# Optimization experiments

Hardware: AMD Instinct MI355X
Metric: run time of the kernel (lower is better)

The kernel has to match this reference:

```python
import jax, jax.numpy as jnp
import numpy as np

T, D, DFF, E, K = 2048, 1024, 2816, 8, 2


def setup_inputs() -> dict:
    key = jax.random.key(0)
    k1, k2, k3, k4, k5, k6 = jax.random.split(key, 6)
    return {
        "x": jax.random.normal(k1, (T, D), dtype=jnp.float32),
        "topk_weight": jax.random.uniform(k2, (T, K), dtype=jnp.float32),
        "gate_w": jax.random.normal(k3, (E, DFF, D), dtype=jnp.float32) * 0.02,
        "up_w": jax.random.normal(k4, (E, DFF, D), dtype=jnp.float32) * 0.02,
        "down_w": jax.random.normal(k5, (E, D, DFF), dtype=jnp.float32) * 0.02,
        "topk_ids": jax.random.randint(k6, (T, K), 0, E, dtype=jnp.int64),
    }


def reference(x, topk_weight, gate_w, up_w, down_w, topk_ids):
    # x: [T, D]; topk_ids/topk_weight: [T, K]
    # Per expert: SwiGLU MLP over all tokens, combined with the per-token
    # routing weight for that expert (0 if the expert was not selected).
    out = jnp.zeros_like(x)
    num_experts = gate_w.shape[0]
    for e in range(num_experts):
        h = jax.nn.silu(x @ gate_w[e].T) * (x @ up_w[e].T)  # [T, DFF]
        y = h @ down_w[e].T                                  # [T, D]
        # sum over top-k slots of routing weight where this expert was chosen
        w_e = jnp.sum(jnp.where(topk_ids == e, topk_weight, 0.0), axis=1)  # [T]
        out = out + y * w_e[:, None]
    return out
```

## Files before the change

### kernel.cpp

```cpp
#include <hip/hip_runtime.h>
#include <stdint.h>

typedef __attribute__((ext_vector_type(8))) __bf16 bf16x8;
typedef __attribute__((ext_vector_type(4))) float f32x4;
typedef __attribute__((ext_vector_type(8))) unsigned short ushort8;

#define T_TOK 2048
#define D_DIM 1024
#define DFF   2816
#define NEXP  8
#define NROWS 4096
#define BK    32
#define NW_ELEM (NEXP * DFF * D_DIM)
#define MAXTM2 24

#define SWZ(r,g) ((g) ^ (((r) >> 1) & 3))

#define TL_N    0
#define TL_BASE 16
#define TL_VAL  80
#define TL_EXP  144

__device__ __forceinline__ void lds_cp16(const void* g, void* l) {
  __builtin_amdgcn_global_load_lds(
      (const __attribute__((address_space(1))) void*)g,
      (__attribute__((address_space(3))) void*)l, 16, 0, 0);
}

__device__ __forceinline__ ushort8 pack_bf16x8(float4 a, float4 b) {
  union { __bf16 h[8]; ushort8 u; } r;
  r.h[0] = (__bf16)a.x; r.h[1] = (__bf16)a.y; r.h[2] = (__bf16)a.z; r.h[3] = (__bf16)a.w;
  r.h[4] = (__bf16)b.x; r.h[5] = (__bf16)b.y; r.h[6] = (__bf16)b.z; r.h[7] = (__bf16)b.w;
  return r.u;
}

__device__ __forceinline__ unsigned short f2bf(float f) {
  union { __bf16 h; unsigned short u; } r;
  r.h = (__bf16)f;
  return r.u;
}

__device__ __forceinline__ float bf2f(unsigned short u) {
  union { uint32_t u; float f; } v; v.u = (uint32_t)u << 16;
  return v.f;
}

__device__ __forceinline__ int xcd_chunk(int bid, int nwork) {
  const int q = nwork >> 3, r = nwork & 7;
  const int xcd = bid & 7;
  const int base = (xcd < r) ? xcd * (q + 1) : r * (q + 1) + (xcd - r) * q;
  return base + (bid >> 3);
}

__global__ __launch_bounds__(512) void routing_kernel(
    const int* __restrict__ ids, const float* __restrict__ w,
    int* __restrict__ cnt, int* __restrict__ off,
    int* __restrict__ tok, float* __restrict__ wgt, int* __restrict__ rowmap,
    int* __restrict__ tl2)
{
  __shared__ int s_cnt[NEXP];
  __shared__ int s_off[NEXP];
  const int lane = threadIdx.x & 63;
  const int e    = threadIdx.x >> 6;

  int total = 0;
  for (int c = 0; c < NROWS / 64; ++c) {
    int id = ids[c * 64 + lane];
    unsigned long long b = __ballot(id == e);
    total += __popcll(b);
  }
  if (lane == 0) s_cnt[e] = total;
  __syncthreads();
  if (threadIdx.x == 0) {
    int acc = 0, n2 = 0;
    for (int i = 0; i < NEXP; ++i) {
      s_off[i] = acc; off[i] = acc; cnt[i] = s_cnt[i];
      for (int j = 0; j < s_cnt[i]; j += 256) {
        tl2[TL_BASE + n2] = acc + j;
        tl2[TL_VAL  + n2] = min(256, s_cnt[i] - j);
        tl2[TL_EXP  + n2] = i;
        ++n2;
      }
      acc += s_cnt[i];
    }
    tl2[TL_N] = n2;
  }
  __syncthreads();
  int base = s_off[e];
  for (int c = 0; c < NROWS / 64; ++c) {
    int idx = c * 64 + lane;
    int id = ids[idx];
    bool m = (id == e);
    unsigned long long b = __ballot(m);
    int pos = __popcll(b & ((1ull << lane) - 1ull));
    if (m) {
      tok[base + pos] = idx >> 1;
      wgt[base + pos] = w[idx];
      rowmap[idx] = base + pos;
    }
    base += __popcll(b);
  }
}

__global__ __launch_bounds__(256) void gather_x_kernel(
    const float* __restrict__ x, const int* __restrict__ tok,
    unsigned short* __restrict__ xg)
{
  const int i = blockIdx.x;
  const int t = tok[i];
  const float4 v = ((const float4*)(x + (size_t)t * D_DIM))[threadIdx.x];
  ushort4 o;
  o.x = f2bf(v.x); o.y = f2bf(v.y); o.z = f2bf(v.z); o.w = f2bf(v.w);
  ((ushort4*)(xg + (size_t)i * D_DIM))[threadIdx.x] = o;
}

__global__ __launch_bounds__(256) void wconv_gu_kernel(
    const float* __restrict__ gw, const float* __restrict__ uw,
    unsigned short* __restrict__ gb, unsigned short* __restrict__ ub)
{
  const size_t n = NW_ELEM / 8;
  const size_t stride = (size_t)gridDim.x * blockDim.x;
  for (size_t i = (size_t)blockIdx.x * blockDim.x + threadIdx.x;
       i < 2 * n; i += stride) {
    const bool up = (i >= n);
    const size_t idx = (up ? i - n : i) * 8;
    const float* src = up ? uw : gw;
    unsigned short* dst = up ? ub : gb;
    float4 a = *(const float4*)(src + idx);
    float4 b = *(const float4*)(src + idx + 4);
    *(ushort8*)(dst + idx) = pack_bf16x8(a, b);
  }
}

#define BM_A 256
#define BN_A 64
#define NT_A (DFF / BN_A)
#define NWORK_A (MAXTM2 * NT_A)
#define WCD_BLKS 1024
#define NWG_A (NWORK_A + WCD_BLKS)
#define KT_A (D_DIM / BK)

__global__ __launch_bounds__(512) void moe_gateup_bf(
    const unsigned short* __restrict__ gbuf, const unsigned short* __restrict__ ubuf,
    const unsigned short* __restrict__ xg, const float* __restrict__ wgt,
    const int* __restrict__ tl2,
    unsigned short* __restrict__ hbuf,
    const float* __restrict__ down_w, unsigned short* __restrict__ dbuf)
{
  const int bid = blockIdx.x;
  const int ntm = tl2[TL_N];
  const int nwork = ntm * NT_A;
  const int tid = threadIdx.x;
  if (bid >= nwork) {
    if (bid >= NWORK_A) {
      const int c = bid - NWORK_A;
      const size_t stride = (size_t)WCD_BLKS * 512;
      for (size_t i = (size_t)c * 512 + tid; i < NW_ELEM / 8; i += stride) {
        const size_t idx = i * 8;
        float4 a = *(const float4*)(down_w + idx);
        float4 b = *(const float4*)(down_w + idx + 4);
        *(ushort8*)(dbuf + idx) = pack_bf16x8(a, b);
      }
    }
    return;
  }
  const int w = xcd_chunk(bid, nwork);
  const int tile = w / NT_A;
  const int nt   = w % NT_A;
  const int row_base = tl2[TL_BASE + tile];
  const int valid    = tl2[TL_VAL  + tile];
  const int e        = tl2[TL_EXP  + tile];
  const int n0 = nt * BN_A;

  __shared__ __align__(16) unsigned short Alds[3][BM_A * BK];
  __shared__ __align__(16) unsigned short Bg[3][BN_A * BK];
  __shared__ __align__(16) unsigned short Bu[3][BN_A * BK];

  const int lane = tid & 63;
  const int wid = tid >> 6;
  const int wm = wid >> 1, wn = wid & 1;
  const int lhi = lane >> 4, llo = lane & 15;

  f32x4 accg[4][2], accu[4][2];
  #pragma unroll
  for (int i = 0; i < 4; ++i)
    #pragma unroll
    for (int j = 0; j < 2; ++j) {
      accg[i][j] = (f32x4){0.f, 0.f, 0.f, 0.f};
      accu[i][j] = (f32x4){0.f, 0.f, 0.f, 0.f};
    }

  const unsigned short* gb = gbuf + ((size_t)e * DFF + n0) * D_DIM;
  const unsigned short* ub = ubuf + ((size_t)e * DFF + n0) * D_DIM;

  const int ar0 = tid >> 2, ag = tid & 3;
  const int ar1 = ar0 + 128;
  const size_t a_src0 = (size_t)(row_base + min(ar0, valid - 1)) * D_DIM + SWZ(ar0, ag) * 8;
  const size_t a_src1 = (size_t)(row_base + min(ar1, valid - 1)) * D_DIM + SWZ(ar1, ag) * 8;
  const int q2 = tid & 255;
  const int br = q2 >> 2, bg2 = q2 & 3;
  const size_t b_src = (size_t)br * D_DIM + SWZ(br, bg2) * 8;
  const unsigned short* bsrc_base = (tid < 256) ? gb : ub;
  unsigned short* bdst[3];
  bdst[0] = (tid < 256) ? &Bg[0][q2 * 8] : &Bu[0][q2 * 8];
  bdst[1] = (tid < 256) ? &Bg[1][q2 * 8] : &Bu[1][q2 * 8];
  bdst[2] = (tid < 256) ? &Bg[2][q2 * 8] : &Bu[2][q2 * 8];

  lds_cp16(xg + a_src0, &Alds[0][tid * 8]);
  lds_cp16(xg + a_src1, &Alds[0][(tid + 512) * 8]);
  lds_cp16(bsrc_base + b_src, bdst[0]);
  {
    const int k1 = BK;
    lds_cp16(xg + a_src0 + k1, &Alds[1][tid * 8]);
    lds_cp16(xg + a_src1 + k1, &Alds[1][(tid + 512) * 8]);
    lds_cp16(bsrc_base + b_src + k1, bdst[1]);
  }

  int cur = 0;
  for (int t = 0; t < KT_A; ++t) {
    asm volatile("s_waitcnt vmcnt(3)" ::: "memory");
    __builtin_amdgcn_s_barrier();

    const int nb = (cur + 2 >= 3) ? cur - 1 : cur + 2;
    const int kn = (t + 2 < KT_A) ? (t + 2) * BK : 0;
    lds_cp16(xg + a_src0 + kn, &Alds[nb][tid * 8]);
    lds_cp16(xg + a_src1 + kn, &Alds[nb][(tid + 512) * 8]);
    lds_cp16(bsrc_base + b_src + kn, bdst[nb]);

    bf16x8 a[4], bgf[2], buf_[2];
    #pragma unroll
    for (int mi = 0; mi < 4; ++mi) {
      int row = wm * 64 + mi * 16 + llo;
      a[mi] = *(const bf16x8*)&Alds[cur][row * BK + SWZ(row, lhi) * 8];
    }
    #pragma unroll
    for (int ni = 0; ni < 2; ++ni) {
      int row = wn * 32 + ni * 16 + llo;
      bgf[ni]  = *(const bf16x8*)&Bg[cur][row * BK + SWZ(row, lhi) * 8];
      buf_[ni] = *(const bf16x8*)&Bu[cur][row * BK + SWZ(row, lhi) * 8];
    }
    #pragma unroll
    for (int mi = 0; mi < 4; ++mi)
      #pragma unroll
      for (int ni = 0; ni < 2; ++ni) {
        accg[mi][ni] = __builtin_amdgcn_mfma_f32_16x16x32_bf16(a[mi], bgf[ni], accg[mi][ni], 0, 0, 0);
        accu[mi][ni] = __builtin_amdgcn_mfma_f32_16x16x32_bf16(a[mi], buf_[ni], accu[mi][ni], 0, 0, 0);
      }

    cur = (cur + 1 >= 3) ? 0 : cur + 1;
  }

  #pragma unroll
  for (int mi = 0; mi < 4; ++mi) {
    #pragma unroll
    for (int r = 0; r < 4; ++r) {
      int row = wm * 64 + mi * 16 + lhi * 4 + r;
      if (row < valid) {
        int grow = row_base + row;
        float wv = wgt[grow];
        size_t base = (size_t)grow * DFF + n0 + wn * 32;
        #pragma unroll
        for (int ni = 0; ni < 2; ++ni) {
          float g = accg[mi][ni][r];
          float u = accu[mi][ni][r];
          float h = (g / (1.f + __expf(-g))) * u * wv;
          hbuf[base + ni * 16 + llo] = f2bf(h);
        }
      }
    }
  }
}

#define BM_B 256
#define BN_B 128
#define NT_B (D_DIM / BN_B)
#define SLICES_B 4
#define NWT_B (NT_B * SLICES_B)
#define NWG_B (MAXTM2 * NWT_B)

#define PIPE_BARRIER_VM3() do { \
    asm volatile("s_waitcnt vmcnt(3)" ::: "memory"); \
    __builtin_amdgcn_s_barrier(); \
  } while (0)

template <bool USE_YBUF>
__global__ __launch_bounds__(512) void moe_down_bf(
    const unsigned short* __restrict__ dbuf,
    const unsigned short* __restrict__ hbuf,
    const int* __restrict__ tok,
    const int* __restrict__ tl2,
    unsigned short* __restrict__ ybuf, float* __restrict__ out_atomic)
{
  constexpr int KS = DFF / SLICES_B;
  constexpr int KT = KS / BK;

  const int bid = blockIdx.x;
  const int ntm = tl2[TL_N];
  const int nwork = ntm * NWT_B;
  if (bid >= nwork) return;
  const int w = xcd_chunk(bid, nwork);
  const int tile = w / NWT_B;
  const int rr   = w % NWT_B;
  const int nt = rr & 7;
  const int sl = rr >> 3;
  const int row_base = tl2[TL_BASE + tile];
  const int valid    = tl2[TL_VAL  + tile];
  const int e        = tl2[TL_EXP  + tile];
  const int n0 = nt * BN_B;
  const int kbeg = sl * KS;

  __shared__ __align__(16) unsigned short Alds[3][BM_B * BK];
  __shared__ __align__(16) unsigned short Blds[3][BN_B * BK];

  const int tid = threadIdx.x, lane = tid & 63, wid = tid >> 6;
  const int wm = wid >> 1, wn = wid & 1;
  const int lhi = lane >> 4, llo = lane & 15;

  f32x4 acc[4][4];
  #pragma unroll
  for (int i = 0; i < 4; ++i)
    #pragma unroll
    for (int j = 0; j < 4; ++j) acc[i][j] = (f32x4){0.f, 0.f, 0.f, 0.f};

  const unsigned short* db = dbuf + ((size_t)e * D_DIM + n0) * DFF;

  const int ar0 = tid >> 2, ag = tid & 3;
  const int ar1 = ar0 + 128;
  const size_t a_src0 = (size_t)(row_base + min(ar0, valid - 1)) * DFF + SWZ(ar0, ag) * 8;
  const size_t a_src1 = (size_t)(row_base + min(ar1, valid - 1)) * DFF + SWZ(ar1, ag) * 8;
  const int brr = tid >> 2, bgg = tid & 3;
  const size_t b_src = (size_t)brr * DFF + SWZ(brr, bgg) * 8;

  lds_cp16(hbuf + a_src0 + kbeg, &Alds[0][tid * 8]);
  lds_cp16(hbuf + a_src1 + kbeg, &Alds[0][(tid + 512) * 8]);
  lds_cp16(db + b_src + kbeg, &Blds[0][tid * 8]);
  {
    const int k1 = kbeg + BK;
    lds_cp16(hbuf + a_src0 + k1, &Alds[1][tid * 8]);
    lds_cp16(hbuf + a_src1 + k1, &Alds[1][(tid + 512) * 8]);
    lds_cp16(db + b_src + k1, &Blds[1][tid * 8]);
  }

  int cur = 0;
  for (int t = 0; t < KT; ++t) {
    PIPE_BARRIER_VM3();

    const int nb = (cur + 2 >= 3) ? cur - 1 : cur + 2;
    const int kn = kbeg + ((t + 2 < KT) ? (t + 2) * BK : 0);
    lds_cp16(hbuf + a_src0 + kn, &Alds[nb][tid * 8]);
    lds_cp16(hbuf + a_src1 + kn, &Alds[nb][(tid + 512) * 8]);
    lds_cp16(db + b_src + kn, &Blds[nb][tid * 8]);

    bf16x8 a[4], b[4];
    #pragma unroll
    for (int mi = 0; mi < 4; ++mi) {
      int row = wm * 64 + mi * 16 + llo;
      a[mi] = *(const bf16x8*)&Alds[cur][row * BK + SWZ(row, lhi) * 8];
    }
    #pragma unroll
    for (int ni = 0; ni < 4; ++ni) {
      int row = wn * 64 + ni * 16 + llo;
      b[ni] = *(const bf16x8*)&Blds[cur][row * BK + SWZ(row, lhi) * 8];
    }
    #pragma unroll
    for (int mi = 0; mi < 4; ++mi)
      #pragma unroll
      for (int ni = 0; ni < 4; ++ni)
        acc[mi][ni] = __builtin_amdgcn_mfma_f32_16x16x32_bf16(a[mi], b[ni], acc[mi][ni], 0, 0, 0);

    cur = (cur + 1 >= 3) ? 0 : cur + 1;
  }

  #pragma unroll
  for (int mi = 0; mi < 4; ++mi) {
    #pragma unroll
    for (int r = 0; r < 4; ++r) {
      int row = wm * 64 + mi * 16 + lhi * 4 + r;
      if (row < valid) {
        if (USE_YBUF) {
          unsigned short* yp = ybuf + ((size_t)sl * NROWS + row_base + row) * D_DIM + n0 + wn * 64;
          #pragma unroll
          for (int ni = 0; ni < 4; ++ni) yp[ni * 16 + llo] = f2bf(acc[mi][ni][r]);
        } else {
          int tk = tok[row_base + row];
          float* op = out_atomic + (size_t)tk * D_DIM + n0 + wn * 64;
          #pragma unroll
          for (int ni = 0; ni < 4; ++ni) atomicAdd(op + ni * 16 + llo, acc[mi][ni][r]);
        }
      }
    }
  }
}

__global__ __launch_bounds__(256) void combine_kernel(
    const unsigned short* __restrict__ ybuf, const int* __restrict__ rowmap,
    float* __restrict__ out)
{
  const int t = blockIdx.x;
  const int d = threadIdx.x * 4;
  const int r0 = rowmap[t * 2], r1 = rowmap[t * 2 + 1];
  float s0 = 0.f, s1 = 0.f, s2 = 0.f, s3 = 0.f;
  #pragma unroll
  for (int sl = 0; sl < SLICES_B; ++sl) {
    ushort4 a = *(const ushort4*)(ybuf + ((size_t)sl * NROWS + r0) * D_DIM + d);
    ushort4 b = *(const ushort4*)(ybuf + ((size_t)sl * NROWS + r1) * D_DIM + d);
    s0 += bf2f(a.x) + bf2f(b.x);
    s1 += bf2f(a.y) + bf2f(b.y);
    s2 += bf2f(a.z) + bf2f(b.z);
    s3 += bf2f(a.w) + bf2f(b.w);
  }
  float4 s = {s0, s1, s2, s3};
  *(float4*)(out + (size_t)t * D_DIM + d) = s;
}

extern "C" void kernel_launch(void* const* d_in, const int* in_sizes, int n_in,
                              void* d_out, int out_size, void* d_ws, size_t ws_size,
                              hipStream_t stream) {
  const float* x      = (const float*)d_in[0];
  const float* topk_w = (const float*)d_in[1];
  const float* gate_w = (const float*)d_in[2];
  const float* up_w   = (const float*)d_in[3];
  const float* down_w = (const float*)d_in[4];
  const int*   ids    = (const int*)d_in[5];
  float* out = (float*)d_out;

  char* ws = (char*)d_ws;
  int*   cnt    = (int*)(ws + 0);
  int*   off    = (int*)(ws + 32);
  int*   tok    = (int*)(ws + 64);
  float* wgt    = (float*)(ws + 64 + NROWS * 4);
  int*   rowmap = (int*)(ws + 64 + NROWS * 8);
  int*   tl2    = (int*)(ws + 50688);

  const size_t XG_OFF = 65536;
  const size_t XG_SZ  = (size_t)NROWS * D_DIM * 2;
  const size_t HB_OFF = XG_OFF + XG_SZ;
  const size_t HB_SZ  = (size_t)NROWS * DFF * 2;
  const size_t W_SZ   = (size_t)NW_ELEM * 2;
  const size_t GB_OFF = HB_OFF + HB_SZ;
  const size_t UB_OFF = GB_OFF + W_SZ;
  const size_t DB_OFF = UB_OFF + W_SZ;
  const size_t YB_OFF = DB_OFF + W_SZ;
  const size_t YB_SZ  = (size_t)SLICES_B * NROWS * D_DIM * 2;

  unsigned short* xg   = (unsigned short*)(ws + XG_OFF);
  unsigned short* hbuf = (unsigned short*)(ws + HB_OFF);
  unsigned short* gbuf = (unsigned short*)(ws + GB_OFF);
  unsigned short* ubuf = (unsigned short*)(ws + UB_OFF);
  unsigned short* dbuf = (unsigned short*)(ws + DB_OFF);
  unsigned short* ybuf = (unsigned short*)(ws + YB_OFF);

  routing_kernel<<<1, 512, 0, stream>>>(ids, topk_w, cnt, off, tok, wgt, rowmap, tl2);
  gather_x_kernel<<<NROWS, 256, 0, stream>>>(x, tok, xg);
  wconv_gu_kernel<<<8192, 256, 0, stream>>>(gate_w, up_w, gbuf, ubuf);
  moe_gateup_bf<<<NWG_A, 512, 0, stream>>>(gbuf, ubuf, xg, wgt, tl2, hbuf, down_w, dbuf);

  if (ws_size >= YB_OFF + YB_SZ) {
    moe_down_bf<true><<<NWG_B, 512, 0, stream>>>(dbuf, hbuf, tok, tl2, ybuf, nullptr);
    combine_kernel<<<T_TOK, 256, 0, stream>>>(ybuf, rowmap, out);
  } else {
    hipMemsetAsync(d_out, 0, (size_t)out_size * sizeof(float), stream);
    moe_down_bf<false><<<NWG_B, 512, 0, stream>>>(dbuf, hbuf, tok, tl2, nullptr, out);
  }
}
```

Baseline: 240.9 us.

## Fuse gate/up weight bf16 conversion into the gate-up GEMM loader

```diff
diff --git a/kernel.cpp b/kernel.cpp
--- a/kernel.cpp
+++ b/kernel.cpp
@@ -114,24 +114,6 @@
   ((ushort4*)(xg + (size_t)i * D_DIM))[threadIdx.x] = o;
 }
 
-__global__ __launch_bounds__(256) void wconv_gu_kernel(
-    const float* __restrict__ gw, const float* __restrict__ uw,
-    unsigned short* __restrict__ gb, unsigned short* __restrict__ ub)
-{
-  const size_t n = NW_ELEM / 8;
-  const size_t stride = (size_t)gridDim.x * blockDim.x;
-  for (size_t i = (size_t)blockIdx.x * blockDim.x + threadIdx.x;
-       i < 2 * n; i += stride) {
-    const bool up = (i >= n);
-    const size_t idx = (up ? i - n : i) * 8;
-    const float* src = up ? uw : gw;
-    unsigned short* dst = up ? ub : gb;
-    float4 a = *(const float4*)(src + idx);
-    float4 b = *(const float4*)(src + idx + 4);
-    *(ushort8*)(dst + idx) = pack_bf16x8(a, b);
-  }
-}
-
 #define BM_A 256
 #define BN_A 64
 #define NT_A (DFF / BN_A)
@@ -140,8 +122,8 @@
 #define NWG_A (NWORK_A + WCD_BLKS)
 #define KT_A (D_DIM / BK)
 
-__global__ __launch_bounds__(512) void moe_gateup_bf(
-    const unsigned short* __restrict__ gbuf, const unsigned short* __restrict__ ubuf,
+__global__ __launch_bounds__(512) void moe_gateup_f32r(
+    const float* __restrict__ gate_w, const float* __restrict__ up_w,
     const unsigned short* __restrict__ xg, const float* __restrict__ wgt,
     const int* __restrict__ tl2,
     unsigned short* __restrict__ hbuf,
@@ -190,42 +172,50 @@
       accu[i][j] = (f32x4){0.f, 0.f, 0.f, 0.f};
     }
 
-  const unsigned short* gb = gbuf + ((size_t)e * DFF + n0) * D_DIM;
-  const unsigned short* ub = ubuf + ((size_t)e * DFF + n0) * D_DIM;
-
   const int ar0 = tid >> 2, ag = tid & 3;
   const int ar1 = ar0 + 128;
   const size_t a_src0 = (size_t)(row_base + min(ar0, valid - 1)) * D_DIM + SWZ(ar0, ag) * 8;
   const size_t a_src1 = (size_t)(row_base + min(ar1, valid - 1)) * D_DIM + SWZ(ar1, ag) * 8;
+
   const int q2 = tid & 255;
   const int br = q2 >> 2, bg2 = q2 & 3;
-  const size_t b_src = (size_t)br * D_DIM + SWZ(br, bg2) * 8;
-  const unsigned short* bsrc_base = (tid < 256) ? gb : ub;
+  const float* bsrc = ((tid < 256) ? gate_w : up_w)
+                    + ((size_t)e * DFF + n0 + br) * D_DIM + bg2 * 8;
+  const int bws = br * BK + SWZ(br, bg2) * 8;
   unsigned short* bdst[3];
-  bdst[0] = (tid < 256) ? &Bg[0][q2 * 8] : &Bu[0][q2 * 8];
-  bdst[1] = (tid < 256) ? &Bg[1][q2 * 8] : &Bu[1][q2 * 8];
-  bdst[2] = (tid < 256) ? &Bg[2][q2 * 8] : &Bu[2][q2 * 8];
-
+  bdst[0] = (tid < 256) ? &Bg[0][bws] : &Bu[0][bws];
+  bdst[1] = (tid < 256) ? &Bg[1][bws] : &Bu[1][bws];
+  bdst[2] = (tid < 256) ? &Bg[2][bws] : &Bu[2][bws];
+
+  {
+    float4 c0 = *(const float4*)(bsrc);
+    float4 c1 = *(const float4*)(bsrc + 4);
+    *(ushort8*)bdst[0] = pack_bf16x8(c0, c1);
+  }
+  float4 pb0 = *(const float4*)(bsrc + BK);
+  float4 pb1 = *(const float4*)(bsrc + BK + 4);
   lds_cp16(xg + a_src0, &Alds[0][tid * 8]);
   lds_cp16(xg + a_src1, &Alds[0][(tid + 512) * 8]);
-  lds_cp16(bsrc_base + b_src, bdst[0]);
-  {
-    const int k1 = BK;
-    lds_cp16(xg + a_src0 + k1, &Alds[1][tid * 8]);
-    lds_cp16(xg + a_src1 + k1, &Alds[1][(tid + 512) * 8]);
-    lds_cp16(bsrc_base + b_src + k1, bdst[1]);
-  }
+  lds_cp16(xg + a_src0 + BK, &Alds[1][tid * 8]);
+  lds_cp16(xg + a_src1 + BK, &Alds[1][(tid + 512) * 8]);
+  asm volatile("s_waitcnt vmcnt(0) lgkmcnt(0)" ::: "memory");
+  __builtin_amdgcn_s_barrier();
 
   int cur = 0;
   for (int t = 0; t < KT_A; ++t) {
-    asm volatile("s_waitcnt vmcnt(3)" ::: "memory");
+    const int nxt = (cur + 1 >= 3) ? cur - 2 : cur + 1;
+    const int nb  = (cur + 2 >= 3) ? cur - 1 : cur + 2;
+    const int kn2 = (t + 2 < KT_A) ? (t + 2) * BK : 0;
+
+    float4 nb0 = *(const float4*)(bsrc + kn2);
+    float4 nb1 = *(const float4*)(bsrc + kn2 + 4);
+
+    asm volatile("s_waitcnt vmcnt(6) lgkmcnt(0)" ::: "memory");
     __builtin_amdgcn_s_barrier();
 
-    const int nb = (cur + 2 >= 3) ? cur - 1 : cur + 2;
-    const int kn = (t + 2 < KT_A) ? (t + 2) * BK : 0;
-    lds_cp16(xg + a_src0 + kn, &Alds[nb][tid * 8]);
-    lds_cp16(xg + a_src1 + kn, &Alds[nb][(tid + 512) * 8]);
-    lds_cp16(bsrc_base + b_src + kn, bdst[nb]);
+    lds_cp16(xg + a_src0 + kn2, &Alds[nb][tid * 8]);
+    lds_cp16(xg + a_src1 + kn2, &Alds[nb][(tid + 512) * 8]);
+    *(ushort8*)bdst[nxt] = pack_bf16x8(pb0, pb1);
 
     bf16x8 a[4], bgf[2], buf_[2];
     #pragma unroll
@@ -247,6 +237,7 @@
         accu[mi][ni] = __builtin_amdgcn_mfma_f32_16x16x32_bf16(a[mi], buf_[ni], accu[mi][ni], 0, 0, 0);
       }
 
+    pb0 = nb0; pb1 = nb1;
     cur = (cur + 1 >= 3) ? 0 : cur + 1;
   }
 
@@ -437,23 +428,18 @@
   const size_t HB_OFF = XG_OFF + XG_SZ;
   const size_t HB_SZ  = (size_t)NROWS * DFF * 2;
   const size_t W_SZ   = (size_t)NW_ELEM * 2;
-  const size_t GB_OFF = HB_OFF + HB_SZ;
-  const size_t UB_OFF = GB_OFF + W_SZ;
-  const size_t DB_OFF = UB_OFF + W_SZ;
+  const size_t DB_OFF = HB_OFF + HB_SZ;
   const size_t YB_OFF = DB_OFF + W_SZ;
   const size_t YB_SZ  = (size_t)SLICES_B * NROWS * D_DIM * 2;
 
   unsigned short* xg   = (unsigned short*)(ws + XG_OFF);
   unsigned short* hbuf = (unsigned short*)(ws + HB_OFF);
-  unsigned short* gbuf = (unsigned short*)(ws + GB_OFF);
-  unsigned short* ubuf = (unsigned short*)(ws + UB_OFF);
   unsigned short* dbuf = (unsigned short*)(ws + DB_OFF);
   unsigned short* ybuf = (unsigned short*)(ws + YB_OFF);
 
   routing_kernel<<<1, 512, 0, stream>>>(ids, topk_w, cnt, off, tok, wgt, rowmap, tl2);
   gather_x_kernel<<<NROWS, 256, 0, stream>>>(x, tok, xg);
-  wconv_gu_kernel<<<8192, 256, 0, stream>>>(gate_w, up_w, gbuf, ubuf);
-  moe_gateup_bf<<<NWG_A, 512, 0, stream>>>(gbuf, ubuf, xg, wgt, tl2, hbuf, down_w, dbuf);
+  moe_gateup_f32r<<<NWG_A, 512, 0, stream>>>(gate_w, up_w, xg, wgt, tl2, hbuf, down_w, dbuf);
 
   if (ws_size >= YB_OFF + YB_SZ) {
     moe_down_bf<true><<<NWG_B, 512, 0, stream>>>(dbuf, hbuf, tok, tl2, ybuf, nullptr);
```

Result: faster. 231.3 us (-4.0%).
